# Optimization experiments

Hardware: AMD Instinct MI355X
Metric: run time of the kernel (lower is better)

## Reference

```python
import jax, jax.numpy as jnp
import numpy as np

B, T, C, H = 4, 4096, 1024, 64

def setup_inputs() -> dict:
    key = jax.random.key(0)
    k1, k2, k3, k4, k5 = jax.random.split(key, 5)
    scale = 0.02
    return {
        "x": jax.random.normal(k1, (B, T, C), dtype=jnp.float32),
        "head_bias": jax.random.normal(k2, (T, T), dtype=jnp.float32) * 0.1,
        "w_k": jax.random.normal(k3, (C, H), dtype=jnp.float32) * scale,
        "w_q": jax.random.normal(k4, (C, H), dtype=jnp.float32) * scale,
        "w_v": jax.random.normal(k5, (C, H), dtype=jnp.float32) * scale,
    }

def reference(x, head_bias, w_k, w_q, w_v):
    # x: (B,T,C) ; projections: (B,T,H)
    k = jnp.einsum('btc,ch->bth', x, w_k)
    q = jnp.einsum('btc,ch->bth', x, w_q)
    v = jnp.einsum('btc,ch->bth', x, w_v)
    Tq = x.shape[1]
    # scores: (B,T,T) with RPE bias and causal mask
    scores = jnp.einsum('bqh,bkh->bqk', q, k) * (k.shape[-1] ** -0.5)
    scores = scores + head_bias[None, :, :]
    causal = jnp.tril(jnp.ones((Tq, Tq), dtype=bool))
    scores = jnp.where(causal[None, :, :], scores, -jnp.inf)
    weights = jax.nn.softmax(scores, axis=-1)
    out = jnp.einsum('bqk,bkh->bqh', weights, v)
    return out
```

## Files before the change

kernel.cpp:

```cpp
#include <hip/hip_runtime.h>
#include <hip/hip_bf16.h>


#define T_DIM 4096
#define C_DIM 1024
#define CK    256
#define SK    64

typedef __attribute__((ext_vector_type(8))) short s16x8;
typedef __attribute__((ext_vector_type(4))) float f32x4;
typedef __attribute__((ext_vector_type(2))) unsigned int u32x2;
typedef __attribute__((ext_vector_type(4))) unsigned int u32x4;

__device__ __forceinline__ short f2bf(float f) {
    unsigned u = __builtin_bit_cast(unsigned, f);
    u += 0x7FFFu + ((u >> 16) & 1u);
    return (short)(u >> 16);
}
__device__ __forceinline__ unsigned pack2(float a, float b) {
    unsigned ua = __builtin_bit_cast(unsigned, a);
    unsigned ub = __builtin_bit_cast(unsigned, b);
    ua += 0x7FFFu + ((ua >> 16) & 1u);
    ub += 0x7FFFu + ((ub >> 16) & 1u);
    return __builtin_amdgcn_perm(ub, ua, 0x07060302u);
}
__device__ __forceinline__ float bf2f(short s) {
    unsigned u = ((unsigned)(unsigned short)s) << 16;
    return __builtin_bit_cast(float, u);
}
__device__ __forceinline__ int chunk_off(int qt) {
    int g = qt >> 4, r = qt & 15;
    return qt + 8 * g * (g - 1) + r * g;
}
__device__ __forceinline__ void async16(const short* g, short* l) {
    __builtin_amdgcn_global_load_lds(
        (const __attribute__((address_space(1))) unsigned int*)g,
        (__attribute__((address_space(3))) unsigned int*)l, 16, 0, 0);
}

__global__ __launch_bounds__(256) void prep_frag(
    const float* __restrict__ wk, const float* __restrict__ wq,
    const float* __restrict__ wv, short* __restrict__ wfrag)
{
    int ksAll = blockIdx.x, mat = blockIdx.y;
    const float* w = (mat == 0) ? wk : ((mat == 1) ? wq : wv);
    float sc = (mat == 1) ? 0.125f : 1.0f;
    int nt = threadIdx.x >> 6, lane = threadIdx.x & 63;
    int quad = lane >> 4, l15 = lane & 15;
    int h = nt * 16 + l15;
    int cb = ksAll * 32 + quad * 8;
    s16x8 v;
    #pragma unroll
    for (int j = 0; j < 8; ++j) v[j] = f2bf(w[(cb + j) * 64 + h] * sc);
    *(s16x8*)&wfrag[((ksAll * 12 + mat * 4 + nt) * 64 + lane) * 8] = v;
}

union ProjSmem {
    short xs[32][1032];
    struct {
        short comb[2][16][136];
        short vsep[64][40];
    } c;
};

__global__ __launch_bounds__(256, 2) void proj_fused(
    const float* __restrict__ x, const short* __restrict__ wfrag,
    short* __restrict__ qb, short* __restrict__ kfrag, short* __restrict__ vfrag)
{
    __shared__ __align__(16) ProjSmem sm;

    int tid = threadIdx.x;
    int w = tid >> 6, lane = tid & 63;
    int rt = w >> 1, h = w & 1;
    int l15 = lane & 15, quad = lane >> 4;
    int m0 = blockIdx.x * 32;

    s16x8 fA[12], fB[12];
    {
        const s16x8* fb = (const s16x8*)&wfrag[((size_t)(h * 16) * 12 * 64 + lane) * 8];
        #pragma unroll
        for (int f = 0; f < 12; ++f) fA[f] = fb[f * 64];
    }

    #pragma unroll 8
    for (int p = 0; p < 32; ++p) {
        f32x4 v = *(const f32x4*)&x[(size_t)(m0 + p) * C_DIM + tid * 4];
        u32x2 d;
        d[0] = pack2(v[0], v[1]);
        d[1] = pack2(v[2], v[3]);
        *(u32x2*)&sm.xs[p][tid * 4] = d;
    }
    __syncthreads();

    f32x4 acc[12];
    #pragma unroll
    for (int i = 0; i < 12; ++i) acc[i] = (f32x4){0.f, 0.f, 0.f, 0.f};

    #pragma unroll 1
    for (int ks = 0; ks < 16; ks += 2) {
        {
            const s16x8* fb = (const s16x8*)&wfrag[((size_t)(h * 16 + ks + 1) * 12 * 64 + lane) * 8];
            #pragma unroll
            for (int f = 0; f < 12; ++f) fB[f] = fb[f * 64];
        }
        s16x8 af = *(const s16x8*)&sm.xs[rt * 16 + l15][(h * 16 + ks) * 32 + quad * 8];
        #pragma unroll
        for (int f = 0; f < 12; ++f)
            acc[f] = __builtin_amdgcn_mfma_f32_16x16x32_bf16(af, fA[f], acc[f], 0, 0, 0);
        if (ks + 2 < 16) {
            const s16x8* fb = (const s16x8*)&wfrag[((size_t)(h * 16 + ks + 2) * 12 * 64 + lane) * 8];
            #pragma unroll
            for (int f = 0; f < 12; ++f) fA[f] = fb[f * 64];
        }
        s16x8 af2 = *(const s16x8*)&sm.xs[rt * 16 + l15][(h * 16 + ks + 1) * 32 + quad * 8];
        #pragma unroll
        for (int f = 0; f < 12; ++f)
            acc[f] = __builtin_amdgcn_mfma_f32_16x16x32_bf16(af2, fB[f], acc[f], 0, 0, 0);
    }
    __syncthreads();

    if (h == 1) {
        #pragma unroll
        for (int f = 0; f < 8; ++f)
            #pragma unroll
            for (int r = 0; r < 4; ++r)
                sm.c.comb[rt][quad * 4 + r][(f >> 2) * 64 + (f & 3) * 16 + l15] = f2bf(acc[f][r]);
        #pragma unroll
        for (int f = 8; f < 12; ++f)
            #pragma unroll
            for (int r = 0; r < 4; ++r)
                sm.c.vsep[(f & 3) * 16 + l15][rt * 16 + quad * 4 + r] = f2bf(acc[f][r]);
    }
    __syncthreads();
    if (h == 0) {
        #pragma unroll
        for (int f = 0; f < 8; ++f)
            #pragma unroll
            for (int r = 0; r < 4; ++r) {
                int col = (f >> 2) * 64 + (f & 3) * 16 + l15, rr = quad * 4 + r;
                sm.c.comb[rt][rr][col] = f2bf(acc[f][r] + bf2f(sm.c.comb[rt][rr][col]));
            }
        #pragma unroll
        for (int f = 8; f < 12; ++f)
            #pragma unroll
            for (int r = 0; r < 4; ++r) {
                int hh = (f & 3) * 16 + l15, kk = rt * 16 + quad * 4 + r;
                sm.c.vsep[hh][kk] = f2bf(acc[f][r] + bf2f(sm.c.vsep[hh][kk]));
            }
    }
    __syncthreads();

    int b = m0 >> 12, t0 = m0 & 4095;
    int t016 = t0 >> 4, kt32 = t0 >> 5;
    {
        int row = tid >> 3, ch = tid & 7;
        s16x8 v = *(const s16x8*)&sm.c.comb[row >> 4][row & 15][64 + ch * 8];
        *(s16x8*)&qb[(size_t)(m0 + row) * 64 + ch * 8] = v;
    }
    {
        int kt = w & 1, ks = w >> 1;
        s16x8 v = *(const s16x8*)&sm.c.comb[kt][l15][ks * 32 + quad * 8];
        *(s16x8*)&kfrag[(size_t)(((b * 256 + t016 + kt) * 2 + ks) * 64 + lane) * 8] = v;
    }
    {
        int nt = w;
        s16x8 v = *(const s16x8*)&sm.c.vsep[nt * 16 + l15][quad * 8];
        *(s16x8*)&vfrag[(size_t)(((b * 128 + kt32) * 4 + nt) * 64 + lane) * 8] = v;
    }
}

#define STAGE(S, KB, VB) do {                                                 \
    async16(ksrc + (size_t)((S) * 8 + w) * 512 + lane * 8, &KB[w * 512]);     \
    async16(vsrc + (size_t)((S) * 8 + w) * 512 + lane * 8, &VB[w * 512]);     \
} while (0)

#define BIAS2(KREL, D0, D1) do {                                              \
    D0 = *(const f32x4*)&brow[(KREL) + quad * 4];                             \
    D1 = *(const f32x4*)&brow[(KREL) + 16 + quad * 4];                        \
} while (0)

#define SOFT(N, AS, BV, PLO, PHI) do {                                        \
    float _sv[4];                                                             \
    _Pragma("unroll")                                                         \
    for (int _r = 0; _r < 4; ++_r) {                                          \
        _sv[_r] = (AS)[_r] + (BV)[_r];                                        \
        if (mask_on && (kabs + (N) * 16 + quad * 4 + _r > q0 + l15))          \
            _sv[_r] = -__builtin_inff();                                      \
        float _p = __expf(_sv[_r]);                                           \
        _sv[_r] = _p;                                                         \
        l_sum += _p;                                                          \
    }                                                                         \
    PLO = pack2(_sv[0], _sv[1]);                                              \
    PHI = pack2(_sv[2], _sv[3]);                                              \
} while (0)

#define COMPUTEK(KB, VB, KREL, B0, B1) do {                                   \
    int _lt = (((KREL) & 63) >> 4);                               \
    int _lv = (((KREL) & 63) >> 5);                               \
    int kabs = kstart + (KREL);                                               \
    s16x8 _ak0 = *(const s16x8*)&KB[(_lt * 2 + 0) * 512 + lane * 8];          \
    s16x8 _ak1 = *(const s16x8*)&KB[(_lt * 2 + 1) * 512 + lane * 8];          \
    s16x8 _ak2 = *(const s16x8*)&KB[(_lt * 2 + 2) * 512 + lane * 8];          \
    s16x8 _ak3 = *(const s16x8*)&KB[(_lt * 2 + 3) * 512 + lane * 8];          \
    f32x4 _aS0 = (f32x4){0.f, 0.f, 0.f, 0.f};                                 \
    f32x4 _aS1 = (f32x4){0.f, 0.f, 0.f, 0.f};                                 \
    _aS0 = __builtin_amdgcn_mfma_f32_16x16x32_bf16(_ak0, aq0, _aS0, 0, 0, 0); \
    _aS0 = __builtin_amdgcn_mfma_f32_16x16x32_bf16(_ak1, aq1, _aS0, 0, 0, 0); \
    _aS1 = __builtin_amdgcn_mfma_f32_16x16x32_bf16(_ak2, aq0, _aS1, 0, 0, 0); \
    _aS1 = __builtin_amdgcn_mfma_f32_16x16x32_bf16(_ak3, aq1, _aS1, 0, 0, 0); \
    unsigned _p0, _p1, _p2, _p3;                                              \
    SOFT(0, _aS0, B0, _p0, _p1);                                              \
    SOFT(1, _aS1, B1, _p2, _p3);                                              \
    asm("v_permlane32_swap_b32 %0, %1" : "+v"(_p0), "+v"(_p2));               \
    asm("v_permlane16_swap_b32 %0, %1" : "+v"(_p0), "+v"(_p2));               \
    asm("v_permlane32_swap_b32 %0, %1" : "+v"(_p1), "+v"(_p3));               \
    asm("v_permlane16_swap_b32 %0, %1" : "+v"(_p1), "+v"(_p3));               \
    u32x4 _apu = (u32x4){_p0, _p1, _p2, _p3};                                 \
    s16x8 _ap = __builtin_bit_cast(s16x8, _apu);                              \
    s16x8 _bv0 = *(const s16x8*)&VB[(_lv * 4 + 0) * 512 + lane * 8];          \
    s16x8 _bv1 = *(const s16x8*)&VB[(_lv * 4 + 1) * 512 + lane * 8];          \
    s16x8 _bv2 = *(const s16x8*)&VB[(_lv * 4 + 2) * 512 + lane * 8];          \
    s16x8 _bv3 = *(const s16x8*)&VB[(_lv * 4 + 3) * 512 + lane * 8];          \
    accO[0] = __builtin_amdgcn_mfma_f32_16x16x32_bf16(_ap, _bv0, accO[0], 0, 0, 0); \
    accO[1] = __builtin_amdgcn_mfma_f32_16x16x32_bf16(_ap, _bv1, accO[1], 0, 0, 0); \
    accO[2] = __builtin_amdgcn_mfma_f32_16x16x32_bf16(_ap, _bv2, accO[2], 0, 0, 0); \
    accO[3] = __builtin_amdgcn_mfma_f32_16x16x32_bf16(_ap, _bv3, accO[3], 0, 0, 0); \
} while (0)

__global__ __launch_bounds__(512, 4) void flash_part(
    const short* __restrict__ qb, const short* __restrict__ kfrag,
    const short* __restrict__ vfrag, const float* __restrict__ bias,
    short* __restrict__ po)
{
    int g = blockIdx.x;
    int c = blockIdx.y;
    int b = blockIdx.z;
    if (c > (g >> 1)) return;

    __shared__ __align__(16) short klds0[8 * 512];
    __shared__ __align__(16) short klds1[8 * 512];
    __shared__ __align__(16) short vlds0[8 * 512];
    __shared__ __align__(16) short vlds1[8 * 512];

    int tid = threadIdx.x;
    int w = tid >> 6, lane = tid & 63;
    int l15 = lane & 15, quad = lane >> 4;

    int qt = g * 8 + w;
    int q0 = qt * 16;
    int kstart = c * CK;
    int kend = min(kstart + CK, q0 + 16);
    int nk = kend - kstart;
    int nkb = min(CK, 128 * g + 128 - kstart);
    int nsub = (nkb + SK - 1) / SK;
    bool mask_on = (kend > q0);

    const short* ksrc = kfrag + (size_t)((b * 256 + c * 16) * 2) * 512;
    const short* vsrc = vfrag + (size_t)((b * 128 + c * 8) * 4) * 512;

    STAGE(0, klds0, vlds0);
    const short* qrow = qb + (size_t)(b * T_DIM + q0 + l15) * 64;
    s16x8 aq0 = *(const s16x8*)(qrow + quad * 8);
    s16x8 aq1 = *(const s16x8*)(qrow + 32 + quad * 8);
    const float* brow = bias + (size_t)(q0 + l15) * T_DIM + kstart;
    f32x4 bA0, bA1, bB0, bB1;
    BIAS2(0, bA0, bA1);
    BIAS2(32, bB0, bB1);

    float l_sum = 0.f;
    f32x4 accO[4];
    #pragma unroll
    for (int nt = 0; nt < 4; ++nt) accO[nt] = (f32x4){0.f, 0.f, 0.f, 0.f};

    __syncthreads();

    int s = 0, krel = 0;
    while (true) {
        bool hn = (s + 1 < nsub);
        if (hn) STAGE(s + 1, klds1, vlds1);
        if (krel < nk)      COMPUTEK(klds0, vlds0, krel, bA0, bA1);
        if (krel + 64 < nk) BIAS2(krel + 64, bA0, bA1);
        if (krel + 32 < nk) COMPUTEK(klds0, vlds0, krel + 32, bB0, bB1);
        if (krel + 96 < nk) BIAS2(krel + 96, bB0, bB1);
        __syncthreads();
        if (!hn) break;
        ++s; krel += SK;
        bool hn2 = (s + 1 < nsub);
        if (hn2) STAGE(s + 1, klds0, vlds0);
        if (krel < nk)      COMPUTEK(klds1, vlds1, krel, bA0, bA1);
        if (krel + 64 < nk) BIAS2(krel + 64, bA0, bA1);
        if (krel + 32 < nk) COMPUTEK(klds1, vlds1, krel + 32, bB0, bB1);
        if (krel + 96 < nk) BIAS2(krel + 96, bB0, bB1);
        __syncthreads();
        if (!hn2) break;
        ++s; krel += SK;
    }

    l_sum += __shfl_xor(l_sum, 16, 64);
    l_sum += __shfl_xor(l_sum, 32, 64);

    short* base = po + (size_t)((chunk_off(qt) + c) * 4 + b) * 1040;
    #pragma unroll
    for (int nt = 0; nt < 4; ++nt)
        #pragma unroll
        for (int r = 0; r < 4; ++r)
            base[(quad * 4 + r) * 64 + nt * 16 + l15] = f2bf(accO[nt][r]);
    if (quad == 0) base[1024 + l15] = f2bf(l_sum);
}

__global__ __launch_bounds__(256) void flash_reduce(
    const short* __restrict__ po, float* __restrict__ out)
{
    int idx = blockIdx.x * 256 + threadIdx.x;
    int row = idx >> 3, c8 = idx & 7;
    int b = row >> 12, t = row & 4095;
    int qt = t >> 4, rloc = t & 15;
    int nc = (t >> 8) + 1;
    int off = chunk_off(qt);
    float o[8];
    #pragma unroll
    for (int j = 0; j < 8; ++j) o[j] = 0.f;
    float l = 0.f;
    #pragma unroll 1
    for (int cc = 0; cc < nc; ++cc) {
        const short* base = po + (size_t)((off + cc) * 4 + b) * 1040;
        s16x8 v = *(const s16x8*)&base[rloc * 64 + c8 * 8];
        #pragma unroll
        for (int j = 0; j < 8; ++j) o[j] += bf2f(v[j]);
        l += bf2f(base[1024 + rloc]);
    }
    float inv = 1.0f / l;
    f32x4 r0 = (f32x4){o[0] * inv, o[1] * inv, o[2] * inv, o[3] * inv};
    f32x4 r1 = (f32x4){o[4] * inv, o[5] * inv, o[6] * inv, o[7] * inv};
    float* op = &out[(size_t)row * 64 + c8 * 8];
    *(f32x4*)op = r0;
    *(f32x4*)(op + 4) = r1;
}

extern "C" void kernel_launch(void* const* d_in, const int* in_sizes, int n_in,
                              void* d_out, int out_size, void* d_ws, size_t ws_size,
                              hipStream_t stream) {
    (void)in_sizes; (void)n_in; (void)out_size; (void)ws_size;
    const float* x    = (const float*)d_in[0];
    const float* bias = (const float*)d_in[1];
    const float* wk   = (const float*)d_in[2];
    const float* wq   = (const float*)d_in[3];
    const float* wv   = (const float*)d_in[4];
    float* out = (float*)d_out;

    short* wfrag = (short*)d_ws;
    short* qb    = wfrag + 196608;
    short* kfrag = qb + 1048576;
    short* vfrag = kfrag + 1048576;
    short* po    = vfrag + 1048576;

    prep_frag<<<dim3(32, 3), dim3(256), 0, stream>>>(wk, wq, wv, wfrag);
    proj_fused<<<dim3(512), dim3(256), 0, stream>>>(x, wfrag, qb, kfrag, vfrag);
    flash_part<<<dim3(32, 16, 4), dim3(512), 0, stream>>>(qb, kfrag, vfrag, bias, po);
    flash_reduce<<<dim3(512), dim3(256), 0, stream>>>(po, out);
}
```

Baseline: 209.1 us.

## Load K/V fragments directly into registers, dropping LDS staging and block syncs

```diff
diff --git a/kernel.cpp b/kernel.cpp
--- a/kernel.cpp
+++ b/kernel.cpp
@@ -5,7 +5,6 @@
 #define T_DIM 4096
 #define C_DIM 1024
 #define CK    256
-#define SK    64
 
 typedef __attribute__((ext_vector_type(8))) short s16x8;
 typedef __attribute__((ext_vector_type(4))) float f32x4;
@@ -31,11 +30,6 @@
 __device__ __forceinline__ int chunk_off(int qt) {
     int g = qt >> 4, r = qt & 15;
     return qt + 8 * g * (g - 1) + r * g;
-}
-__device__ __forceinline__ void async16(const short* g, short* l) {
-    __builtin_amdgcn_global_load_lds(
-        (const __attribute__((address_space(1))) unsigned int*)g,
-        (__attribute__((address_space(3))) unsigned int*)l, 16, 0, 0);
 }
 
 __global__ __launch_bounds__(256) void prep_frag(
@@ -169,9 +163,20 @@
     }
 }
 
-#define STAGE(S, KB, VB) do {                                                 \
-    async16(ksrc + (size_t)((S) * 8 + w) * 512 + lane * 8, &KB[w * 512]);     \
-    async16(vsrc + (size_t)((S) * 8 + w) * 512 + lane * 8, &VB[w * 512]);     \
+#define LOADK(AK, KREL) do {                                                  \
+    const short* _p = kfb + (size_t)(((KREL) >> 4) * 2) * 512 + lane * 8;     \
+    AK[0] = *(const s16x8*)_p;                                                \
+    AK[1] = *(const s16x8*)(_p + 512);                                        \
+    AK[2] = *(const s16x8*)(_p + 1024);                                       \
+    AK[3] = *(const s16x8*)(_p + 1536);                                       \
+} while (0)
+
+#define LOADV(BV, KREL) do {                                                  \
+    const short* _p = vfb + (size_t)(((KREL) >> 5) * 4) * 512 + lane * 8;     \
+    BV[0] = *(const s16x8*)_p;                                                \
+    BV[1] = *(const s16x8*)(_p + 512);                                        \
+    BV[2] = *(const s16x8*)(_p + 1024);                                       \
+    BV[3] = *(const s16x8*)(_p + 1536);                                       \
 } while (0)
 
 #define BIAS2(KREL, D0, D1) do {                                              \
@@ -194,20 +199,14 @@
     PHI = pack2(_sv[2], _sv[3]);                                              \
 } while (0)
 
-#define COMPUTEK(KB, VB, KREL, B0, B1) do {                                   \
-    int _lt = (((KREL) & 63) >> 4);                               \
-    int _lv = (((KREL) & 63) >> 5);                               \
+#define COMPUTE(AK, BV, KREL, B0, B1) do {                                    \
     int kabs = kstart + (KREL);                                               \
-    s16x8 _ak0 = *(const s16x8*)&KB[(_lt * 2 + 0) * 512 + lane * 8];          \
-    s16x8 _ak1 = *(const s16x8*)&KB[(_lt * 2 + 1) * 512 + lane * 8];          \
-    s16x8 _ak2 = *(const s16x8*)&KB[(_lt * 2 + 2) * 512 + lane * 8];          \
-    s16x8 _ak3 = *(const s16x8*)&KB[(_lt * 2 + 3) * 512 + lane * 8];          \
     f32x4 _aS0 = (f32x4){0.f, 0.f, 0.f, 0.f};                                 \
     f32x4 _aS1 = (f32x4){0.f, 0.f, 0.f, 0.f};                                 \
-    _aS0 = __builtin_amdgcn_mfma_f32_16x16x32_bf16(_ak0, aq0, _aS0, 0, 0, 0); \
-    _aS0 = __builtin_amdgcn_mfma_f32_16x16x32_bf16(_ak1, aq1, _aS0, 0, 0, 0); \
-    _aS1 = __builtin_amdgcn_mfma_f32_16x16x32_bf16(_ak2, aq0, _aS1, 0, 0, 0); \
-    _aS1 = __builtin_amdgcn_mfma_f32_16x16x32_bf16(_ak3, aq1, _aS1, 0, 0, 0); \
+    _aS0 = __builtin_amdgcn_mfma_f32_16x16x32_bf16(AK[0], aq0, _aS0, 0, 0, 0); \
+    _aS0 = __builtin_amdgcn_mfma_f32_16x16x32_bf16(AK[1], aq1, _aS0, 0, 0, 0); \
+    _aS1 = __builtin_amdgcn_mfma_f32_16x16x32_bf16(AK[2], aq0, _aS1, 0, 0, 0); \
+    _aS1 = __builtin_amdgcn_mfma_f32_16x16x32_bf16(AK[3], aq1, _aS1, 0, 0, 0); \
     unsigned _p0, _p1, _p2, _p3;                                              \
     SOFT(0, _aS0, B0, _p0, _p1);                                              \
     SOFT(1, _aS1, B1, _p2, _p3);                                              \
@@ -217,17 +216,13 @@
     asm("v_permlane16_swap_b32 %0, %1" : "+v"(_p1), "+v"(_p3));               \
     u32x4 _apu = (u32x4){_p0, _p1, _p2, _p3};                                 \
     s16x8 _ap = __builtin_bit_cast(s16x8, _apu);                              \
-    s16x8 _bv0 = *(const s16x8*)&VB[(_lv * 4 + 0) * 512 + lane * 8];          \
-    s16x8 _bv1 = *(const s16x8*)&VB[(_lv * 4 + 1) * 512 + lane * 8];          \
-    s16x8 _bv2 = *(const s16x8*)&VB[(_lv * 4 + 2) * 512 + lane * 8];          \
-    s16x8 _bv3 = *(const s16x8*)&VB[(_lv * 4 + 3) * 512 + lane * 8];          \
-    accO[0] = __builtin_amdgcn_mfma_f32_16x16x32_bf16(_ap, _bv0, accO[0], 0, 0, 0); \
-    accO[1] = __builtin_amdgcn_mfma_f32_16x16x32_bf16(_ap, _bv1, accO[1], 0, 0, 0); \
-    accO[2] = __builtin_amdgcn_mfma_f32_16x16x32_bf16(_ap, _bv2, accO[2], 0, 0, 0); \
-    accO[3] = __builtin_amdgcn_mfma_f32_16x16x32_bf16(_ap, _bv3, accO[3], 0, 0, 0); \
-} while (0)
-
-__global__ __launch_bounds__(512, 4) void flash_part(
+    accO[0] = __builtin_amdgcn_mfma_f32_16x16x32_bf16(_ap, BV[0], accO[0], 0, 0, 0); \
+    accO[1] = __builtin_amdgcn_mfma_f32_16x16x32_bf16(_ap, BV[1], accO[1], 0, 0, 0); \
+    accO[2] = __builtin_amdgcn_mfma_f32_16x16x32_bf16(_ap, BV[2], accO[2], 0, 0, 0); \
+    accO[3] = __builtin_amdgcn_mfma_f32_16x16x32_bf16(_ap, BV[3], accO[3], 0, 0, 0); \
+} while (0)
+
+__global__ __launch_bounds__(256, 4) void flash_part(
     const short* __restrict__ qb, const short* __restrict__ kfrag,
     const short* __restrict__ vfrag, const float* __restrict__ bias,
     short* __restrict__ po)
@@ -235,65 +230,47 @@
     int g = blockIdx.x;
     int c = blockIdx.y;
     int b = blockIdx.z;
-    if (c > (g >> 1)) return;
-
-    __shared__ __align__(16) short klds0[8 * 512];
-    __shared__ __align__(16) short klds1[8 * 512];
-    __shared__ __align__(16) short vlds0[8 * 512];
-    __shared__ __align__(16) short vlds1[8 * 512];
+    if (c > (g >> 2)) return;
 
     int tid = threadIdx.x;
     int w = tid >> 6, lane = tid & 63;
     int l15 = lane & 15, quad = lane >> 4;
 
-    int qt = g * 8 + w;
+    int qt = g * 4 + w;
     int q0 = qt * 16;
     int kstart = c * CK;
     int kend = min(kstart + CK, q0 + 16);
     int nk = kend - kstart;
-    int nkb = min(CK, 128 * g + 128 - kstart);
-    int nsub = (nkb + SK - 1) / SK;
     bool mask_on = (kend > q0);
 
-    const short* ksrc = kfrag + (size_t)((b * 256 + c * 16) * 2) * 512;
-    const short* vsrc = vfrag + (size_t)((b * 128 + c * 8) * 4) * 512;
-
-    STAGE(0, klds0, vlds0);
+    const short* kfb = kfrag + (size_t)((b * 256 + c * 16) * 2) * 512;
+    const short* vfb = vfrag + (size_t)((b * 128 + c * 8) * 4) * 512;
+    const float* brow = bias + (size_t)(q0 + l15) * T_DIM + kstart;
+
+    s16x8 akA[4], akB[4], bvA[4], bvB[4];
+    f32x4 bA0, bA1, bB0, bB1;
+    LOADK(akA, 0);
+    LOADV(bvA, 0);
+    BIAS2(0, bA0, bA1);
     const short* qrow = qb + (size_t)(b * T_DIM + q0 + l15) * 64;
     s16x8 aq0 = *(const s16x8*)(qrow + quad * 8);
     s16x8 aq1 = *(const s16x8*)(qrow + 32 + quad * 8);
-    const float* brow = bias + (size_t)(q0 + l15) * T_DIM + kstart;
-    f32x4 bA0, bA1, bB0, bB1;
-    BIAS2(0, bA0, bA1);
-    BIAS2(32, bB0, bB1);
 
     float l_sum = 0.f;
     f32x4 accO[4];
     #pragma unroll
     for (int nt = 0; nt < 4; ++nt) accO[nt] = (f32x4){0.f, 0.f, 0.f, 0.f};
 
-    __syncthreads();
-
-    int s = 0, krel = 0;
+    int krel = 0;
     while (true) {
-        bool hn = (s + 1 < nsub);
-        if (hn) STAGE(s + 1, klds1, vlds1);
-        if (krel < nk)      COMPUTEK(klds0, vlds0, krel, bA0, bA1);
-        if (krel + 64 < nk) BIAS2(krel + 64, bA0, bA1);
-        if (krel + 32 < nk) COMPUTEK(klds0, vlds0, krel + 32, bB0, bB1);
-        if (krel + 96 < nk) BIAS2(krel + 96, bB0, bB1);
-        __syncthreads();
-        if (!hn) break;
-        ++s; krel += SK;
-        bool hn2 = (s + 1 < nsub);
-        if (hn2) STAGE(s + 1, klds0, vlds0);
-        if (krel < nk)      COMPUTEK(klds1, vlds1, krel, bA0, bA1);
-        if (krel + 64 < nk) BIAS2(krel + 64, bA0, bA1);
-        if (krel + 32 < nk) COMPUTEK(klds1, vlds1, krel + 32, bB0, bB1);
-        if (krel + 96 < nk) BIAS2(krel + 96, bB0, bB1);
-        __syncthreads();
-        if (!hn2) break;
-        ++s; krel += SK;
+        int kp = krel + 32; if (kp > CK - 32) kp = CK - 32;
+        LOADK(akB, kp); LOADV(bvB, kp); BIAS2(kp, bB0, bB1);
+        COMPUTE(akA, bvA, krel, bA0, bA1);
+        krel += 32; if (krel >= nk) break;
+        kp = krel + 32; if (kp > CK - 32) kp = CK - 32;
+        LOADK(akA, kp); LOADV(bvA, kp); BIAS2(kp, bA0, bA1);
+        COMPUTE(akB, bvB, krel, bB0, bB1);
+        krel += 32; if (krel >= nk) break;
     }
 
     l_sum += __shfl_xor(l_sum, 16, 64);
@@ -356,6 +333,6 @@
 
     prep_frag<<<dim3(32, 3), dim3(256), 0, stream>>>(wk, wq, wv, wfrag);
     proj_fused<<<dim3(512), dim3(256), 0, stream>>>(x, wfrag, qb, kfrag, vfrag);
-    flash_part<<<dim3(32, 16, 4), dim3(512), 0, stream>>>(qb, kfrag, vfrag, bias, po);
+    flash_part<<<dim3(64, 16, 4), dim3(256), 0, stream>>>(qb, kfrag, vfrag, bias, po);
     flash_reduce<<<dim3(512), dim3(256), 0, stream>>>(po, out);
 }
```

New measurement: 221.9 us. 6.1% more time.
